# Kernel optimization log

Measured on AMD Instinct MI355X. Metric: run time of the kernel, lower is better.

## Reference

```python
import jax, jax.numpy as jnp
import numpy as np

B, S, D = 4, 2048, 1024

def setup_inputs() -> dict:
    key = jax.random.key(0)
    ks = jax.random.split(key, 7)
    scale = 1.0 / np.sqrt(D)
    return {
        "x": jax.random.normal(ks[0], (B, S, D), dtype=jnp.float32),
        "Wq": jax.random.uniform(ks[1], (D, D), jnp.float32, -scale, scale),
        "bq": jax.random.uniform(ks[2], (D,), jnp.float32, -scale, scale),
        "Wk": jax.random.uniform(ks[3], (D, D), jnp.float32, -scale, scale),
        "bk": jax.random.uniform(ks[4], (D,), jnp.float32, -scale, scale),
        "Wv": jax.random.uniform(ks[5], (D, D), jnp.float32, -scale, scale),
        "bv": jax.random.uniform(ks[6], (D,), jnp.float32, -scale, scale),
    }

def reference(x, Wq, bq, Wk, bk, Wv, bv):
    # Linear layers: x @ W^T + b (torch nn.Linear convention)
    q = jnp.einsum('bsd,ed->bse', x, Wq) + bq  # [B,S,D]
    k = jnp.einsum('bsd,ed->bse', x, Wk) + bk
    v = jnp.einsum('bsd,ed->bse', x, Wv) + bv
    inv_sqrt_d = 1.0 / jnp.sqrt(jnp.asarray(k.shape[-1], k.dtype))
    scores = jnp.einsum('bqd,bkd->bqk', q, k) * inv_sqrt_d  # [B,S,S]
    attn = jax.nn.softmax(scores, axis=-1)
    return jnp.einsum('bqk,bkd->bqd', attn, v)
```

## Files before the change

### kernel.cpp

```cpp
#include <hip/hip_runtime.h>
#include <cstdint>


typedef __bf16 bf16x8_t __attribute__((ext_vector_type(8)));
typedef float  f32x4_t  __attribute__((ext_vector_type(4)));
typedef int    i32x8_t  __attribute__((ext_vector_type(8)));
typedef int    i32x4_t  __attribute__((ext_vector_type(4)));

__device__ __forceinline__ uint16_t f2bf(float f) {
    union { float f; uint32_t u; } v; v.f = f;
    return (uint16_t)((v.u + 0x7fffu + ((v.u >> 16) & 1u)) >> 16);
}

__device__ __forceinline__ uint8_t f2fp8(float f) {
    union { float f; uint32_t u; } v; v.f = f;
    const uint32_t sgn = (v.u >> 31) << 7;
    const uint32_t mag = v.u & 0x7fffffffu;
    uint32_t out;
    if (mag < 0x3c800000u) {
        out = (uint32_t)__builtin_rintf(__builtin_fabsf(f) * 512.0f);
    } else {
        uint32_t t = mag + 0x7ffffu + ((mag >> 20) & 1u);
        out = (t >> 20) - 960u;
        if (out > 0x7eu) out = 0x7eu;
    }
    return (uint8_t)(sgn | out);
}

__device__ __forceinline__ void gload_lds16(const void* g, void* lds) {
    __builtin_amdgcn_global_load_lds(
        (const __attribute__((address_space(1))) void*)g,
        (__attribute__((address_space(3))) void*)lds, 16, 0, 0);
}

#define BAR()   asm volatile("s_barrier" ::: "memory")
#define WLGKM() asm volatile("s_waitcnt lgkmcnt(0)" ::: "memory")

template <int BN, int EPI, typename OutT>
__global__ __launch_bounds__(512, 2) void gemm8p(
    const uint16_t* __restrict__ A, int lda, long long sAz,
    const uint16_t* __restrict__ B, int ldb, long long sBz,
    OutT* __restrict__ C, int ldc, long long sCz,
    const float* __restrict__ bias0, const float* __restrict__ bias1,
    const float* __restrict__ gsum, int K)
{
    constexpr int NF    = BN / 64;
    constexpr int LB    = BN / 128;
    constexpr int BSLOT = BN * 128;
    constexpr int BKH   = BN * 64;

    __shared__ uint16_t ldsA[32768];
    __shared__ uint16_t ldsB[BN * 128];
    __shared__ float    inv_denom[256];

    const int tid  = threadIdx.x;
    const int wv   = tid >> 6;
    const int lane = tid & 63;
    const int quad = lane >> 4;
    const int l15  = lane & 15;
    const int wm   = wv >> 2;
    const int wn   = wv & 3;
    const int z    = blockIdx.z;

    A += (long long)z * sAz;
    B += (long long)z * sBz;
    C += (long long)z * sCz;

    const int m0 = blockIdx.x * 256;
    const int n0 = blockIdx.y * BN;

    if (EPI == 4) {
        if (tid < 256) {
            const float* gp = gsum + (long long)z * 32768 + (m0 + tid) * 16;
            float s = 0.f;
#pragma unroll
            for (int t = 0; t < 16; ++t) s += gp[t];
            inv_denom[tid] = 1.f / s;
        }
    }

    const int r  = tid >> 2;
    const int ca = (tid & 3) ^ ((tid >> 4) & 3);
    const uint16_t* aS = A + (long long)(m0 + r) * lda + ca * 8;
    const uint16_t* bS = B + (long long)(n0 + r) * ldb + ca * 8;
    const int dOf = wv * 1024;

    auto STAGE_A = [&](int kt, int h, int sl) {
        const uint16_t* s = aS + kt * 64 + h * 32;
        char* d = (char*)ldsA + sl * 32768 + h * 16384 + dOf;
        gload_lds16(s, d);
        gload_lds16(s + (long long)128 * lda, d + 8192);
    };
    auto STAGE_B = [&](int kt, int h, int sl) {
        const uint16_t* s = bS + kt * 64 + h * 32;
        char* d = (char*)ldsB + sl * BSLOT + h * BKH + dOf;
        gload_lds16(s, d);
        if (LB == 2) gload_lds16(s + (long long)128 * ldb, d + 8192);
    };

    const int csw  = ((quad ^ (l15 >> 2)) & 3) * 16;
    const int aOff = (wm * 128 + l15) * 64 + csw;
    const int bOff = (wn * (BN / 4) + l15) * 64 + csw;

    f32x4_t acc[8][NF];
#pragma unroll
    for (int i = 0; i < 8; ++i)
#pragma unroll
        for (int j = 0; j < NF; ++j) acc[i][j] = f32x4_t{0.f, 0.f, 0.f, 0.f};

    const int NT = K >> 6;

    STAGE_B(0, 0, 0); STAGE_A(0, 0, 0); STAGE_B(0, 1, 0); STAGE_A(0, 1, 0);
    STAGE_B(1, 0, 1); STAGE_A(1, 0, 1); STAGE_B(1, 1, 1);
    if constexpr (LB == 2) asm volatile("s_waitcnt vmcnt(6)" ::: "memory");
    else                   asm volatile("s_waitcnt vmcnt(4)" ::: "memory");
    BAR();

    for (int t = 0; t < NT; ++t) {
        const int sl = t & 1;
        const int so = sl ^ 1;
        const int t1 = (t + 1 < NT) ? t + 1 : 0;
        const int t2 = (t + 2 < NT) ? t + 2 : 0;
        const char* Ab = (const char*)ldsA + sl * 32768;
        const char* Bb = (const char*)ldsB + sl * BSLOT;

        bf16x8_t af[4], bfv[NF];

#pragma unroll
        for (int i = 0; i < 4; ++i)
            af[i] = *(const bf16x8_t*)(Ab + i * 1024 + aOff);
#pragma unroll
        for (int j = 0; j < NF; ++j)
            bfv[j] = *(const bf16x8_t*)(Bb + j * 1024 + bOff);
        STAGE_A(t1, 1, so);
        BAR(); WLGKM();
        __builtin_amdgcn_s_setprio(1);
#pragma unroll
        for (int i = 0; i < 4; ++i)
#pragma unroll
            for (int j = 0; j < NF; ++j)
                acc[i][j] = __builtin_amdgcn_mfma_f32_16x16x32_bf16(
                    af[i], bfv[j], acc[i][j], 0, 0, 0);
        __builtin_amdgcn_s_setprio(0);
        BAR();

#pragma unroll
        for (int i = 0; i < 4; ++i)
            af[i] = *(const bf16x8_t*)(Ab + 4096 + i * 1024 + aOff);
        STAGE_B(t2, 0, sl);
        BAR(); WLGKM();
        __builtin_amdgcn_s_setprio(1);
#pragma unroll
        for (int i = 0; i < 4; ++i)
#pragma unroll
            for (int j = 0; j < NF; ++j)
                acc[4 + i][j] = __builtin_amdgcn_mfma_f32_16x16x32_bf16(
                    af[i], bfv[j], acc[4 + i][j], 0, 0, 0);
        __builtin_amdgcn_s_setprio(0);
        BAR();

#pragma unroll
        for (int i = 0; i < 4; ++i)
            af[i] = *(const bf16x8_t*)(Ab + 16384 + i * 1024 + aOff);
#pragma unroll
        for (int j = 0; j < NF; ++j)
            bfv[j] = *(const bf16x8_t*)(Bb + BKH + j * 1024 + bOff);
        STAGE_A(t2, 0, sl);
        BAR(); WLGKM();
        __builtin_amdgcn_s_setprio(1);
#pragma unroll
        for (int i = 0; i < 4; ++i)
#pragma unroll
            for (int j = 0; j < NF; ++j)
                acc[i][j] = __builtin_amdgcn_mfma_f32_16x16x32_bf16(
                    af[i], bfv[j], acc[i][j], 0, 0, 0);
        __builtin_amdgcn_s_setprio(0);
        BAR();

#pragma unroll
        for (int i = 0; i < 4; ++i)
            af[i] = *(const bf16x8_t*)(Ab + 16384 + 4096 + i * 1024 + aOff);
        STAGE_B(t2, 1, sl);
        BAR(); WLGKM();
        __builtin_amdgcn_s_setprio(1);
#pragma unroll
        for (int i = 0; i < 4; ++i)
#pragma unroll
            for (int j = 0; j < NF; ++j)
                acc[4 + i][j] = __builtin_amdgcn_mfma_f32_16x16x32_bf16(
                    af[i], bfv[j], acc[4 + i][j], 0, 0, 0);
        __builtin_amdgcn_s_setprio(0);
        if constexpr (LB == 2) asm volatile("s_waitcnt vmcnt(6)" ::: "memory");
        else                   asm volatile("s_waitcnt vmcnt(4)" ::: "memory");
        BAR();
    }

    if (EPI == 1 || EPI == 2) {
        const float* bias = (z == 0) ? bias0 : bias1;
#pragma unroll
        for (int fi = 0; fi < 8; ++fi) {
            const int mb = m0 + wm * 128 + fi * 16 + quad * 4;
            float rb[4];
            if (EPI == 2) {
#pragma unroll
                for (int rr = 0; rr < 4; ++rr) rb[rr] = bias[mb + rr];
            }
#pragma unroll
            for (int fj = 0; fj < NF; ++fj) {
                const int n = n0 + wn * (BN / 4) + fj * 16 + l15;
                const float cb = (EPI == 1) ? bias[n] : 0.f;
#pragma unroll
                for (int rr = 0; rr < 4; ++rr) {
                    const float vv = acc[fi][fj][rr] + ((EPI == 1) ? cb : rb[rr]);
                    if (sizeof(OutT) == 1)
                        ((uint8_t*)C)[(long long)(mb + rr) * ldc + n] = f2fp8(vv);
                    else
                        ((uint16_t*)C)[(long long)(mb + rr) * ldc + n] = f2bf(vv);
                }
            }
        }
    } else {
#pragma unroll
        for (int fi = 0; fi < 8; ++fi) {
            const int rl = wm * 128 + fi * 16 + quad * 4;
            const int mb = m0 + rl;
#pragma unroll
            for (int fj = 0; fj < NF; ++fj) {
                const int n = n0 + wn * (BN / 4) + fj * 16 + l15;
#pragma unroll
                for (int rr = 0; rr < 4; ++rr)
                    ((float*)C)[(long long)(mb + rr) * ldc + n] =
                        acc[fi][fj][rr] * inv_denom[rl + rr];
            }
        }
    }
}

__global__ __launch_bounds__(256, 3) void score_f8(
    const uint8_t* __restrict__ Qf8, const uint8_t* __restrict__ Kf8,
    uint16_t* __restrict__ P, float* __restrict__ gsum, float alpha)
{
    __shared__ uint8_t ldsA[128 * 128];
    __shared__ uint8_t ldsB[128 * 128];

    const int tid  = threadIdx.x;
    const int wave = tid >> 6;
    const int lane = tid & 63;
    const int quad = lane >> 4;
    const int l15  = lane & 15;
    const int z    = blockIdx.z;

    const uint8_t* A = Qf8 + (long long)z * 2097152;
    const uint8_t* B = Kf8 + (long long)z * 2097152;
    uint16_t* C = P + (long long)z * 4194304;

    const int m0 = blockIdx.x * 128;
    const int n0 = blockIdx.y * 128;

    const uint8_t* gA[4];
    const uint8_t* gB[4];
    uint8_t* lA[4];
    uint8_t* lB[4];
#pragma unroll
    for (int c = 0; c < 4; ++c) {
        const int s   = (c * 4 + wave) * 64 + lane;
        const int r   = s >> 3;
        const int col = ((s & 7) ^ (r & 7)) * 16;
        gA[c] = A + (long long)(m0 + r) * 1024 + col;
        gB[c] = B + (long long)(n0 + r) * 1024 + col;
        lA[c] = ldsA + (c * 4 + wave) * 1024;
        lB[c] = ldsB + (c * 4 + wave) * 1024;
    }

    const int m_off = (wave & 1) * 64;
    const int n_off = (wave >> 1) * 64;

    f32x4_t acc[4][4];
#pragma unroll
    for (int i = 0; i < 4; ++i)
#pragma unroll
        for (int j = 0; j < 4; ++j)
            acc[i][j] = f32x4_t{0.f, 0.f, 0.f, 0.f};

    const int h0 = quad * 2;
    const int h1 = quad * 2 + 1;

    for (int k0 = 0; k0 < 1024; k0 += 128) {
#pragma unroll
        for (int c = 0; c < 4; ++c) gload_lds16(gA[c], lA[c]);
#pragma unroll
        for (int c = 0; c < 4; ++c) gload_lds16(gB[c], lB[c]);
#pragma unroll
        for (int c = 0; c < 4; ++c) { gA[c] += 128; gB[c] += 128; }
        __syncthreads();

        i32x8_t af[4], bfr[4];
#pragma unroll
        for (int i = 0; i < 4; ++i) {
            const int m = m_off + i * 16 + l15;
            const int sw = m & 7;
            const i32x4_t lo = *(const i32x4_t*)(ldsA + m * 128 + (h0 ^ sw) * 16);
            const i32x4_t hi = *(const i32x4_t*)(ldsA + m * 128 + (h1 ^ sw) * 16);
            af[i] = i32x8_t{lo[0], lo[1], lo[2], lo[3], hi[0], hi[1], hi[2], hi[3]};
        }
#pragma unroll
        for (int j = 0; j < 4; ++j) {
            const int n = n_off + j * 16 + l15;
            const int sw = n & 7;
            const i32x4_t lo = *(const i32x4_t*)(ldsB + n * 128 + (h0 ^ sw) * 16);
            const i32x4_t hi = *(const i32x4_t*)(ldsB + n * 128 + (h1 ^ sw) * 16);
            bfr[j] = i32x8_t{lo[0], lo[1], lo[2], lo[3], hi[0], hi[1], hi[2], hi[3]};
        }
#pragma unroll
        for (int i = 0; i < 4; ++i)
#pragma unroll
            for (int j = 0; j < 4; ++j)
                acc[i][j] = __builtin_amdgcn_mfma_scale_f32_16x16x128_f8f6f4(
                    af[i], bfr[j], acc[i][j],
                    0, 0,
                    0, 0x7f7f7f7f,
                    0, 0x7f7f7f7f);
        __syncthreads();
    }

    float rs[4][4];
#pragma unroll
    for (int i = 0; i < 4; ++i)
#pragma unroll
        for (int r = 0; r < 4; ++r) rs[i][r] = 0.f;
#pragma unroll
    for (int i = 0; i < 4; ++i) {
        const int mb = m0 + m_off + i * 16 + quad * 4;
#pragma unroll
        for (int j = 0; j < 4; ++j) {
            const int n = n0 + n_off + j * 16 + l15;
#pragma unroll
            for (int r = 0; r < 4; ++r) {
                const float e = exp2f(acc[i][j][r] * alpha);
                rs[i][r] += e;
                C[(long long)(mb + r) * 2048 + n] = f2bf(e);
            }
        }
    }
#pragma unroll
    for (int m = 1; m < 16; m <<= 1)
#pragma unroll
        for (int i = 0; i < 4; ++i)
#pragma unroll
            for (int r = 0; r < 4; ++r)
                rs[i][r] += __shfl_xor(rs[i][r], m);
    float* lp = (float*)ldsA;
    if (l15 == 0) {
#pragma unroll
        for (int i = 0; i < 4; ++i)
#pragma unroll
            for (int r = 0; r < 4; ++r)
                lp[wave * 64 + i * 16 + quad * 4 + r] = rs[i][r];
    }
    __syncthreads();
    if (tid < 128) {
        const float s = lp[(tid >> 6) * 64 + (tid & 63)] +
                        lp[((tid >> 6) + 2) * 64 + (tid & 63)];
        gsum[(long long)z * 32768 + (m0 + tid) * 16 + blockIdx.y] = s;
    }
}

__global__ void cvt_all(const float* __restrict__ x,
                        const float* __restrict__ Wq, const float* __restrict__ Wk,
                        const float* __restrict__ Wv,
                        uint16_t* __restrict__ x_bf, uint16_t* __restrict__ w_bf) {
    const int b = blockIdx.x;
    const float* src;
    uint16_t* dst;
    int i;
    if (b < 8192) {
        src = x; dst = x_bf; i = b * 256 + threadIdx.x;
    } else {
        const int wz = (b - 8192) >> 10;
        const int rb = (b - 8192) & 1023;
        src = (wz == 0) ? Wq : (wz == 1) ? Wk : Wv;
        dst = w_bf + (long long)wz * 1048576;
        i = rb * 256 + threadIdx.x;
    }
    const float4 f = ((const float4*)src)[i];
    ushort4 o;
    o.x = f2bf(f.x); o.y = f2bf(f.y); o.z = f2bf(f.z); o.w = f2bf(f.w);
    ((ushort4*)dst)[i] = o;
}

extern "C" void kernel_launch(void* const* d_in, const int* in_sizes, int n_in,
                              void* d_out, int out_size, void* d_ws, size_t ws_size,
                              hipStream_t stream) {
    const float* x  = (const float*)d_in[0];
    const float* Wq = (const float*)d_in[1];
    const float* bq = (const float*)d_in[2];
    const float* Wk = (const float*)d_in[3];
    const float* bk = (const float*)d_in[4];
    const float* Wv = (const float*)d_in[5];
    const float* bv = (const float*)d_in[6];
    float* out = (float*)d_out;

    char* w = (char*)d_ws;
    uint16_t* x_bf = (uint16_t*)(w);
    float*    gsum = (float*)(w);
    uint16_t* w_bf = (uint16_t*)(w + 16777216);
    uint8_t*  Qf8  = (uint8_t*)(w + 23068672);
    uint8_t*  Kf8  = (uint8_t*)(w + 31457280);
    uint16_t* Vt   = (uint16_t*)(w + 39845888);
    uint16_t* Pb   = (uint16_t*)(w + 56623104);

    cvt_all<<<11264, 256, 0, stream>>>(x, Wq, Wk, Wv, x_bf, w_bf);

    gemm8p<256, 1, uint8_t><<<dim3(32, 4, 2), 512, 0, stream>>>(
        x_bf, 1024, 0LL,
        w_bf, 1024, 1048576LL,
        Qf8, 1024, 8388608LL,
        bq, bk, nullptr, 1024);

    gemm8p<128, 2, uint16_t><<<dim3(4, 64, 1), 512, 0, stream>>>(
        w_bf + 2097152, 1024, 0LL,
        x_bf, 1024, 0LL,
        Vt, 8192, 0LL,
        bv, bv, nullptr, 1024);

    score_f8<<<dim3(16, 16, 4), 256, 0, stream>>>(
        Qf8, Kf8, Pb, gsum, 0.045084222f);

    gemm8p<128, 4, float><<<dim3(8, 8, 4), 512, 0, stream>>>(
        Pb, 2048, 4194304LL,
        Vt, 8192, 2048LL,
        out, 1024, 2097152LL,
        nullptr, nullptr, gsum, 2048);
}
```

Before: 260.6 us.

## Split GEMM mainloop by NF with two-phase schedule for narrow tiles, tweak LDS swizzle

```diff
diff --git a/kernel.cpp b/kernel.cpp
--- a/kernel.cpp
+++ b/kernel.cpp
@@ -80,7 +80,7 @@
     }
 
     const int r  = tid >> 2;
-    const int ca = (tid & 3) ^ ((tid >> 4) & 3);
+    const int ca = (tid & 3) ^ ((tid >> 3) & 3);
     const uint16_t* aS = A + (long long)(m0 + r) * lda + ca * 8;
     const uint16_t* bS = B + (long long)(n0 + r) * ldb + ca * 8;
     const int dOf = wv * 1024;
@@ -98,7 +98,7 @@
         if (LB == 2) gload_lds16(s + (long long)128 * ldb, d + 8192);
     };
 
-    const int csw  = ((quad ^ (l15 >> 2)) & 3) * 16;
+    const int csw  = ((quad ^ (l15 >> 1)) & 3) * 16;
     const int aOff = (wm * 128 + l15) * 64 + csw;
     const int bOff = (wn * (BN / 4) + l15) * 64 + csw;
 
@@ -110,89 +110,145 @@
 
     const int NT = K >> 6;
 
-    STAGE_B(0, 0, 0); STAGE_A(0, 0, 0); STAGE_B(0, 1, 0); STAGE_A(0, 1, 0);
-    STAGE_B(1, 0, 1); STAGE_A(1, 0, 1); STAGE_B(1, 1, 1);
-    if constexpr (LB == 2) asm volatile("s_waitcnt vmcnt(6)" ::: "memory");
-    else                   asm volatile("s_waitcnt vmcnt(4)" ::: "memory");
-    BAR();
-
-    for (int t = 0; t < NT; ++t) {
-        const int sl = t & 1;
-        const int so = sl ^ 1;
-        const int t1 = (t + 1 < NT) ? t + 1 : 0;
-        const int t2 = (t + 2 < NT) ? t + 2 : 0;
-        const char* Ab = (const char*)ldsA + sl * 32768;
-        const char* Bb = (const char*)ldsB + sl * BSLOT;
-
-        bf16x8_t af[4], bfv[NF];
-
-#pragma unroll
-        for (int i = 0; i < 4; ++i)
-            af[i] = *(const bf16x8_t*)(Ab + i * 1024 + aOff);
-#pragma unroll
-        for (int j = 0; j < NF; ++j)
-            bfv[j] = *(const bf16x8_t*)(Bb + j * 1024 + bOff);
-        STAGE_A(t1, 1, so);
-        BAR(); WLGKM();
-        __builtin_amdgcn_s_setprio(1);
-#pragma unroll
-        for (int i = 0; i < 4; ++i)
-#pragma unroll
-            for (int j = 0; j < NF; ++j)
-                acc[i][j] = __builtin_amdgcn_mfma_f32_16x16x32_bf16(
-                    af[i], bfv[j], acc[i][j], 0, 0, 0);
-        __builtin_amdgcn_s_setprio(0);
+    if constexpr (NF == 4) {
+        STAGE_B(0, 0, 0); STAGE_A(0, 0, 0); STAGE_B(0, 1, 0); STAGE_A(0, 1, 0);
+        STAGE_B(1, 0, 1); STAGE_A(1, 0, 1); STAGE_B(1, 1, 1);
+        asm volatile("s_waitcnt vmcnt(6)" ::: "memory");
         BAR();
 
-#pragma unroll
-        for (int i = 0; i < 4; ++i)
-            af[i] = *(const bf16x8_t*)(Ab + 4096 + i * 1024 + aOff);
-        STAGE_B(t2, 0, sl);
-        BAR(); WLGKM();
-        __builtin_amdgcn_s_setprio(1);
-#pragma unroll
-        for (int i = 0; i < 4; ++i)
-#pragma unroll
-            for (int j = 0; j < NF; ++j)
-                acc[4 + i][j] = __builtin_amdgcn_mfma_f32_16x16x32_bf16(
-                    af[i], bfv[j], acc[4 + i][j], 0, 0, 0);
-        __builtin_amdgcn_s_setprio(0);
+        for (int t = 0; t < NT; ++t) {
+            const int sl = t & 1;
+            const int so = sl ^ 1;
+            const int t1 = (t + 1 < NT) ? t + 1 : 0;
+            const int t2 = (t + 2 < NT) ? t + 2 : 0;
+            const char* Ab = (const char*)ldsA + sl * 32768;
+            const char* Bb = (const char*)ldsB + sl * BSLOT;
+
+            bf16x8_t af[4], bfv[4];
+
+#pragma unroll
+            for (int i = 0; i < 4; ++i)
+                af[i] = *(const bf16x8_t*)(Ab + i * 1024 + aOff);
+#pragma unroll
+            for (int j = 0; j < 4; ++j)
+                bfv[j] = *(const bf16x8_t*)(Bb + j * 1024 + bOff);
+            STAGE_A(t1, 1, so);
+            BAR(); WLGKM();
+            __builtin_amdgcn_s_setprio(1);
+#pragma unroll
+            for (int i = 0; i < 4; ++i)
+#pragma unroll
+                for (int j = 0; j < 4; ++j)
+                    acc[i][j] = __builtin_amdgcn_mfma_f32_16x16x32_bf16(
+                        af[i], bfv[j], acc[i][j], 0, 0, 0);
+            __builtin_amdgcn_s_setprio(0);
+            BAR();
+
+#pragma unroll
+            for (int i = 0; i < 4; ++i)
+                af[i] = *(const bf16x8_t*)(Ab + 4096 + i * 1024 + aOff);
+            STAGE_B(t2, 0, sl);
+            BAR(); WLGKM();
+            __builtin_amdgcn_s_setprio(1);
+#pragma unroll
+            for (int i = 0; i < 4; ++i)
+#pragma unroll
+                for (int j = 0; j < 4; ++j)
+                    acc[4 + i][j] = __builtin_amdgcn_mfma_f32_16x16x32_bf16(
+                        af[i], bfv[j], acc[4 + i][j], 0, 0, 0);
+            __builtin_amdgcn_s_setprio(0);
+            BAR();
+
+#pragma unroll
+            for (int i = 0; i < 4; ++i)
+                af[i] = *(const bf16x8_t*)(Ab + 16384 + i * 1024 + aOff);
+#pragma unroll
+            for (int j = 0; j < 4; ++j)
+                bfv[j] = *(const bf16x8_t*)(Bb + BKH + j * 1024 + bOff);
+            STAGE_A(t2, 0, sl);
+            BAR(); WLGKM();
+            __builtin_amdgcn_s_setprio(1);
+#pragma unroll
+            for (int i = 0; i < 4; ++i)
+#pragma unroll
+                for (int j = 0; j < 4; ++j)
+                    acc[i][j] = __builtin_amdgcn_mfma_f32_16x16x32_bf16(
+                        af[i], bfv[j], acc[i][j], 0, 0, 0);
+            __builtin_amdgcn_s_setprio(0);
+            BAR();
+
+#pragma unroll
+            for (int i = 0; i < 4; ++i)
+                af[i] = *(const bf16x8_t*)(Ab + 16384 + 4096 + i * 1024 + aOff);
+            STAGE_B(t2, 1, sl);
+            BAR(); WLGKM();
+            __builtin_amdgcn_s_setprio(1);
+#pragma unroll
+            for (int i = 0; i < 4; ++i)
+#pragma unroll
+                for (int j = 0; j < 4; ++j)
+                    acc[4 + i][j] = __builtin_amdgcn_mfma_f32_16x16x32_bf16(
+                        af[i], bfv[j], acc[4 + i][j], 0, 0, 0);
+            __builtin_amdgcn_s_setprio(0);
+            asm volatile("s_waitcnt vmcnt(6)" ::: "memory");
+            BAR();
+        }
+    } else {
+        static_assert(NF != 2 || LB == 1, "pair = 3 loads assumes LB==1");
+        STAGE_A(0, 0, 0); STAGE_B(0, 0, 0);
+        STAGE_A(0, 1, 0); STAGE_B(0, 1, 0);
+        STAGE_A(1, 0, 1); STAGE_B(1, 0, 1);
+        asm volatile("s_waitcnt vmcnt(6)" ::: "memory");
         BAR();
 
-#pragma unroll
-        for (int i = 0; i < 4; ++i)
-            af[i] = *(const bf16x8_t*)(Ab + 16384 + i * 1024 + aOff);
-#pragma unroll
-        for (int j = 0; j < NF; ++j)
-            bfv[j] = *(const bf16x8_t*)(Bb + BKH + j * 1024 + bOff);
-        STAGE_A(t2, 0, sl);
-        BAR(); WLGKM();
-        __builtin_amdgcn_s_setprio(1);
-#pragma unroll
-        for (int i = 0; i < 4; ++i)
-#pragma unroll
-            for (int j = 0; j < NF; ++j)
-                acc[i][j] = __builtin_amdgcn_mfma_f32_16x16x32_bf16(
-                    af[i], bfv[j], acc[i][j], 0, 0, 0);
-        __builtin_amdgcn_s_setprio(0);
-        BAR();
-
-#pragma unroll
-        for (int i = 0; i < 4; ++i)
-            af[i] = *(const bf16x8_t*)(Ab + 16384 + 4096 + i * 1024 + aOff);
-        STAGE_B(t2, 1, sl);
-        BAR(); WLGKM();
-        __builtin_amdgcn_s_setprio(1);
-#pragma unroll
-        for (int i = 0; i < 4; ++i)
-#pragma unroll
-            for (int j = 0; j < NF; ++j)
-                acc[4 + i][j] = __builtin_amdgcn_mfma_f32_16x16x32_bf16(
-                    af[i], bfv[j], acc[4 + i][j], 0, 0, 0);
-        __builtin_amdgcn_s_setprio(0);
-        if constexpr (LB == 2) asm volatile("s_waitcnt vmcnt(6)" ::: "memory");
-        else                   asm volatile("s_waitcnt vmcnt(4)" ::: "memory");
-        BAR();
+        for (int t = 0; t < NT; ++t) {
+            const int sl = t & 1;
+            const int so = sl ^ 1;
+            const int t1 = (t + 1 < NT) ? t + 1 : 0;
+            const int t2 = (t + 2 < NT) ? t + 2 : 0;
+            const char* Ab = (const char*)ldsA + sl * 32768;
+            const char* Bb = (const char*)ldsB + sl * BSLOT;
+
+            bf16x8_t af[8], bfv[2];
+
+#pragma unroll
+            for (int i = 0; i < 8; ++i)
+                af[i] = *(const bf16x8_t*)(Ab + i * 1024 + aOff);
+#pragma unroll
+            for (int j = 0; j < 2; ++j)
+                bfv[j] = *(const bf16x8_t*)(Bb + j * 1024 + bOff);
+            STAGE_A(t1, 1, so); STAGE_B(t1, 1, so);
+            BAR(); WLGKM();
+            __builtin_amdgcn_s_setprio(1);
+#pragma unroll
+            for (int i = 0; i < 8; ++i)
+#pragma unroll
+                for (int j = 0; j < 2; ++j)
+                    acc[i][j] = __builtin_amdgcn_mfma_f32_16x16x32_bf16(
+                        af[i], bfv[j], acc[i][j], 0, 0, 0);
+            __builtin_amdgcn_s_setprio(0);
+            asm volatile("s_waitcnt vmcnt(6)" ::: "memory");
+            BAR();
+
+#pragma unroll
+            for (int i = 0; i < 8; ++i)
+                af[i] = *(const bf16x8_t*)(Ab + 16384 + i * 1024 + aOff);
+#pragma unroll
+            for (int j = 0; j < 2; ++j)
+                bfv[j] = *(const bf16x8_t*)(Bb + BKH + j * 1024 + bOff);
+            STAGE_A(t2, 0, sl); STAGE_B(t2, 0, sl);
+            BAR(); WLGKM();
+            __builtin_amdgcn_s_setprio(1);
+#pragma unroll
+            for (int i = 0; i < 8; ++i)
+#pragma unroll
+                for (int j = 0; j < 2; ++j)
+                    acc[i][j] = __builtin_amdgcn_mfma_f32_16x16x32_bf16(
+                        af[i], bfv[j], acc[i][j], 0, 0, 0);
+            __builtin_amdgcn_s_setprio(0);
+            asm volatile("s_waitcnt vmcnt(6)" ::: "memory");
+            BAR();
+        }
     }
 
     if (EPI == 1 || EPI == 2) {
```

Result: faster. 251.6 us (-3.5%).

## Restructure GEMM main loop into two phases with fixed 128-wide N tile

Applied to the files above, without the earlier changes.

```diff
diff --git a/kernel.cpp b/kernel.cpp
--- a/kernel.cpp
+++ b/kernel.cpp
@@ -36,21 +36,18 @@
 #define BAR()   asm volatile("s_barrier" ::: "memory")
 #define WLGKM() asm volatile("s_waitcnt lgkmcnt(0)" ::: "memory")
 
-template <int BN, int EPI, typename OutT>
-__global__ __launch_bounds__(512, 2) void gemm8p(
+template <int EPI, typename OutT>
+__global__ __launch_bounds__(512, 2) void gemm2p(
     const uint16_t* __restrict__ A, int lda, long long sAz,
     const uint16_t* __restrict__ B, int ldb, long long sBz,
     OutT* __restrict__ C, int ldc, long long sCz,
     const float* __restrict__ bias0, const float* __restrict__ bias1,
     const float* __restrict__ gsum, int K)
 {
-    constexpr int NF    = BN / 64;
-    constexpr int LB    = BN / 128;
-    constexpr int BSLOT = BN * 128;
-    constexpr int BKH   = BN * 64;
+    constexpr int BN = 128;
 
     __shared__ uint16_t ldsA[32768];
-    __shared__ uint16_t ldsB[BN * 128];
+    __shared__ uint16_t ldsB[16384];
     __shared__ float    inv_denom[256];
 
     const int tid  = threadIdx.x;
@@ -80,7 +77,7 @@
     }
 
     const int r  = tid >> 2;
-    const int ca = (tid & 3) ^ ((tid >> 4) & 3);
+    const int ca = (tid & 3) ^ ((tid >> 3) & 3);
     const uint16_t* aS = A + (long long)(m0 + r) * lda + ca * 8;
     const uint16_t* bS = B + (long long)(n0 + r) * ldb + ca * 8;
     const int dOf = wv * 1024;
@@ -93,27 +90,26 @@
     };
     auto STAGE_B = [&](int kt, int h, int sl) {
         const uint16_t* s = bS + kt * 64 + h * 32;
-        char* d = (char*)ldsB + sl * BSLOT + h * BKH + dOf;
+        char* d = (char*)ldsB + sl * 16384 + h * 8192 + dOf;
         gload_lds16(s, d);
-        if (LB == 2) gload_lds16(s + (long long)128 * ldb, d + 8192);
     };
 
-    const int csw  = ((quad ^ (l15 >> 2)) & 3) * 16;
+    const int csw  = ((quad ^ (l15 >> 1)) & 3) * 16;
     const int aOff = (wm * 128 + l15) * 64 + csw;
-    const int bOff = (wn * (BN / 4) + l15) * 64 + csw;
-
-    f32x4_t acc[8][NF];
+    const int bOff = (wn * 32 + l15) * 64 + csw;
+
+    f32x4_t acc[8][2];
 #pragma unroll
     for (int i = 0; i < 8; ++i)
 #pragma unroll
-        for (int j = 0; j < NF; ++j) acc[i][j] = f32x4_t{0.f, 0.f, 0.f, 0.f};
+        for (int j = 0; j < 2; ++j) acc[i][j] = f32x4_t{0.f, 0.f, 0.f, 0.f};
 
     const int NT = K >> 6;
 
-    STAGE_B(0, 0, 0); STAGE_A(0, 0, 0); STAGE_B(0, 1, 0); STAGE_A(0, 1, 0);
-    STAGE_B(1, 0, 1); STAGE_A(1, 0, 1); STAGE_B(1, 1, 1);
-    if constexpr (LB == 2) asm volatile("s_waitcnt vmcnt(6)" ::: "memory");
-    else                   asm volatile("s_waitcnt vmcnt(4)" ::: "memory");
+    STAGE_A(0, 0, 0); STAGE_B(0, 0, 0);
+    STAGE_A(0, 1, 0); STAGE_B(0, 1, 0);
+    STAGE_A(1, 0, 1); STAGE_B(1, 0, 1);
+    asm volatile("s_waitcnt vmcnt(6)" ::: "memory");
     BAR();
 
     for (int t = 0; t < NT; ++t) {
@@ -122,76 +118,46 @@
         const int t1 = (t + 1 < NT) ? t + 1 : 0;
         const int t2 = (t + 2 < NT) ? t + 2 : 0;
         const char* Ab = (const char*)ldsA + sl * 32768;
-        const char* Bb = (const char*)ldsB + sl * BSLOT;
-
-        bf16x8_t af[4], bfv[NF];
-
-#pragma unroll
-        for (int i = 0; i < 4; ++i)
+        const char* Bb = (const char*)ldsB + sl * 16384;
+
+        bf16x8_t af[8], bfv[2];
+
+#pragma unroll
+        for (int i = 0; i < 8; ++i)
             af[i] = *(const bf16x8_t*)(Ab + i * 1024 + aOff);
 #pragma unroll
-        for (int j = 0; j < NF; ++j)
+        for (int j = 0; j < 2; ++j)
             bfv[j] = *(const bf16x8_t*)(Bb + j * 1024 + bOff);
-        STAGE_A(t1, 1, so);
+        STAGE_A(t1, 1, so); STAGE_B(t1, 1, so);
         BAR(); WLGKM();
         __builtin_amdgcn_s_setprio(1);
 #pragma unroll
-        for (int i = 0; i < 4; ++i)
-#pragma unroll
-            for (int j = 0; j < NF; ++j)
+        for (int i = 0; i < 8; ++i)
+#pragma unroll
+            for (int j = 0; j < 2; ++j)
                 acc[i][j] = __builtin_amdgcn_mfma_f32_16x16x32_bf16(
                     af[i], bfv[j], acc[i][j], 0, 0, 0);
         __builtin_amdgcn_s_setprio(0);
+        asm volatile("s_waitcnt vmcnt(6)" ::: "memory");
         BAR();
 
 #pragma unroll
-        for (int i = 0; i < 4; ++i)
-            af[i] = *(const bf16x8_t*)(Ab + 4096 + i * 1024 + aOff);
-        STAGE_B(t2, 0, sl);
+        for (int i = 0; i < 8; ++i)
+            af[i] = *(const bf16x8_t*)(Ab + 16384 + i * 1024 + aOff);
+#pragma unroll
+        for (int j = 0; j < 2; ++j)
+            bfv[j] = *(const bf16x8_t*)(Bb + 8192 + j * 1024 + bOff);
+        STAGE_A(t2, 0, sl); STAGE_B(t2, 0, sl);
         BAR(); WLGKM();
         __builtin_amdgcn_s_setprio(1);
 #pragma unroll
-        for (int i = 0; i < 4; ++i)
-#pragma unroll
-            for (int j = 0; j < NF; ++j)
-                acc[4 + i][j] = __builtin_amdgcn_mfma_f32_16x16x32_bf16(
-                    af[i], bfv[j], acc[4 + i][j], 0, 0, 0);
-        __builtin_amdgcn_s_setprio(0);
-        BAR();
-
-#pragma unroll
-        for (int i = 0; i < 4; ++i)
-            af[i] = *(const bf16x8_t*)(Ab + 16384 + i * 1024 + aOff);
-#pragma unroll
-        for (int j = 0; j < NF; ++j)
-            bfv[j] = *(const bf16x8_t*)(Bb + BKH + j * 1024 + bOff);
-        STAGE_A(t2, 0, sl);
-        BAR(); WLGKM();
-        __builtin_amdgcn_s_setprio(1);
-#pragma unroll
-        for (int i = 0; i < 4; ++i)
-#pragma unroll
-            for (int j = 0; j < NF; ++j)
+        for (int i = 0; i < 8; ++i)
+#pragma unroll
+            for (int j = 0; j < 2; ++j)
                 acc[i][j] = __builtin_amdgcn_mfma_f32_16x16x32_bf16(
                     af[i], bfv[j], acc[i][j], 0, 0, 0);
         __builtin_amdgcn_s_setprio(0);
-        BAR();
-
-#pragma unroll
-        for (int i = 0; i < 4; ++i)
-            af[i] = *(const bf16x8_t*)(Ab + 16384 + 4096 + i * 1024 + aOff);
-        STAGE_B(t2, 1, sl);
-        BAR(); WLGKM();
-        __builtin_amdgcn_s_setprio(1);
-#pragma unroll
-        for (int i = 0; i < 4; ++i)
-#pragma unroll
-            for (int j = 0; j < NF; ++j)
-                acc[4 + i][j] = __builtin_amdgcn_mfma_f32_16x16x32_bf16(
-                    af[i], bfv[j], acc[4 + i][j], 0, 0, 0);
-        __builtin_amdgcn_s_setprio(0);
-        if constexpr (LB == 2) asm volatile("s_waitcnt vmcnt(6)" ::: "memory");
-        else                   asm volatile("s_waitcnt vmcnt(4)" ::: "memory");
+        asm volatile("s_waitcnt vmcnt(6)" ::: "memory");
         BAR();
     }
 
@@ -206,8 +172,8 @@
                 for (int rr = 0; rr < 4; ++rr) rb[rr] = bias[mb + rr];
             }
 #pragma unroll
-            for (int fj = 0; fj < NF; ++fj) {
-                const int n = n0 + wn * (BN / 4) + fj * 16 + l15;
+            for (int fj = 0; fj < 2; ++fj) {
+                const int n = n0 + wn * 32 + fj * 16 + l15;
                 const float cb = (EPI == 1) ? bias[n] : 0.f;
 #pragma unroll
                 for (int rr = 0; rr < 4; ++rr) {
@@ -225,8 +191,8 @@
             const int rl = wm * 128 + fi * 16 + quad * 4;
             const int mb = m0 + rl;
 #pragma unroll
-            for (int fj = 0; fj < NF; ++fj) {
-                const int n = n0 + wn * (BN / 4) + fj * 16 + l15;
+            for (int fj = 0; fj < 2; ++fj) {
+                const int n = n0 + wn * 32 + fj * 16 + l15;
 #pragma unroll
                 for (int rr = 0; rr < 4; ++rr)
                     ((float*)C)[(long long)(mb + rr) * ldc + n] =
@@ -411,13 +377,13 @@
 
     cvt_all<<<11264, 256, 0, stream>>>(x, Wq, Wk, Wv, x_bf, w_bf);
 
-    gemm8p<256, 1, uint8_t><<<dim3(32, 4, 2), 512, 0, stream>>>(
+    gemm2p<1, uint8_t><<<dim3(32, 8, 2), 512, 0, stream>>>(
         x_bf, 1024, 0LL,
         w_bf, 1024, 1048576LL,
         Qf8, 1024, 8388608LL,
         bq, bk, nullptr, 1024);
 
-    gemm8p<128, 2, uint16_t><<<dim3(4, 64, 1), 512, 0, stream>>>(
+    gemm2p<2, uint16_t><<<dim3(4, 64, 1), 512, 0, stream>>>(
         w_bf + 2097152, 1024, 0LL,
         x_bf, 1024, 0LL,
         Vt, 8192, 0LL,
@@ -426,7 +392,7 @@
     score_f8<<<dim3(16, 16, 4), 256, 0, stream>>>(
         Qf8, Kf8, Pb, gsum, 0.045084222f);
 
-    gemm8p<128, 4, float><<<dim3(8, 8, 4), 512, 0, stream>>>(
+    gemm2p<4, float><<<dim3(8, 8, 4), 512, 0, stream>>>(
         Pb, 2048, 4194304LL,
         Vt, 8192, 2048LL,
         out, 1024, 2097152LL,
```

After: 250.9 us. -3.7%, faster.
